# Optimization experiments

Measured on AMD Instinct MI355X. Metric: run time of the kernel, lower is better.

Reference implementation:

```python
import jax, jax.numpy as jnp
import numpy as np

N_PATCHES = 4
PATCH = 64  # image_size // n_patches = 256 // 4
GROUPS = 32
EPS = 1e-5


def setup_inputs() -> dict:
    key = jax.random.key(0)
    k1, k2 = jax.random.split(key)
    x = jax.random.normal(k1, (8, 128, 256, 256), dtype=jnp.float32)
    y = jax.random.normal(k2, (8, 128, 256, 256), dtype=jnp.float32)
    # GroupNorm affine params (torch default init: weight=1, bias=0)
    weight = jnp.ones((128,), dtype=jnp.float32)
    bias = jnp.zeros((128,), dtype=jnp.float32)
    return {"x": x, "y": y, "weight": weight, "bias": bias}


def reference(x, y, weight, bias):
    b, c, h, w = x.shape
    n, p, g = N_PATCHES, PATCH, GROUPS
    cg = c // g
    # extract patches: (b, c, n, p, n, p) -> (b, i, j, c, hp, wp)
    xp = x.reshape(b, c, n, p, n, p).transpose(0, 2, 4, 1, 3, 5)
    yp = y.reshape(b, c, n, p, n, p).transpose(0, 2, 4, 1, 3, 5)
    # per-patch GroupNorm in float32 (GroupNorm.forward casts to float)
    xg = xp.astype(jnp.float32).reshape(b, n, n, g, cg, p, p)
    mean = xg.mean(axis=(4, 5, 6), keepdims=True)
    var = xg.var(axis=(4, 5, 6), keepdims=True)
    xn = (xg - mean) * jax.lax.rsqrt(var + EPS)
    xn = xn.reshape(b, n, n, c, p, p)
    xn = xn * weight[:, None, None] + bias[:, None, None]
    xn = xn.astype(x.dtype)
    # silu-gated scale, shift = 0
    out = xn * (1.0 + jax.nn.silu(yp))
    # reassemble: (b, i, j, c, hp, wp) -> (b, c, i, hp, j, wp) -> (b, c, H, W)
    out = out.transpose(0, 3, 1, 4, 2, 5).reshape(b, c, h, w)
    return out
```

## Files before the change

### kernel.cpp

```cpp
#include <hip/hip_runtime.h>


constexpr int CHANNELS = 128;
constexpr int HW = 256;
constexpr int NP = 4;
constexpr int G = 32;
constexpr int CPG = CHANNELS / G;
constexpr float EPS = 1e-5f;

typedef float f32x4 __attribute__((ext_vector_type(4)));

__device__ __forceinline__ float fast_gate(float v) {
    const float e = __builtin_amdgcn_exp2f(v * -1.44269504088896f);
    return 1.0f + v * __builtin_amdgcn_rcpf(1.0f + e);
}

__global__ __launch_bounds__(512, 4)
void gn_patch_gate_kernel(const float* __restrict__ x,
                          const float* __restrict__ y,
                          const float* __restrict__ wgt,
                          const float* __restrict__ bvec,
                          float* __restrict__ out)
{
    __shared__ float4 xs[4096];
    __shared__ float red[16];

    const int bid = blockIdx.x;
    const int g  = bid & 31;
    const int pj = (bid >> 5) & 3;
    const int pi = (bid >> 7) & 3;
    const int b  = bid >> 9;
    const int tid = threadIdx.x;

    const unsigned cstride = HW * HW;
    const unsigned base =
        (((unsigned)b * CHANNELS + (unsigned)g * CPG) * HW + (unsigned)pi * 64) * HW
        + (unsigned)pj * 64;

    float y0[8], y1[8], y2[8], y3[8];
    unsigned addr[8];
    float s = 0.f, ss = 0.f;
#pragma unroll
    for (int k = 0; k < 8; ++k) {
        const unsigned u  = (unsigned)tid + (unsigned)(k << 9);
        const unsigned cc = u >> 10;
        const unsigned r  = (u >> 4) & 63;
        const unsigned c4 = u & 15;
        const unsigned a  = base + cc * cstride + r * HW + (c4 << 2);
        addr[k] = a;
        const float4 v = *reinterpret_cast<const float4*>(x + a);
        const float4 w = *reinterpret_cast<const float4*>(y + a);
        float w0 = w.x, w1 = w.y, w2 = w.z, w3 = w.w;
        asm volatile("" : "+v"(w0), "+v"(w1), "+v"(w2), "+v"(w3));
        y0[k] = w0; y1[k] = w1; y2[k] = w2; y3[k] = w3;
        xs[u] = v;
        s  += (v.x + v.y) + (v.z + v.w);
        ss += (v.x * v.x + v.y * v.y) + (v.z * v.z + v.w * v.w);
    }

#pragma unroll
    for (int off = 32; off; off >>= 1) {
        s  += __shfl_xor(s, off);
        ss += __shfl_xor(ss, off);
    }
    const int wv = tid >> 6;
    if ((tid & 63) == 0) { red[wv] = s; red[8 + wv] = ss; }
    __syncthreads();
    float ts = 0.f, tss = 0.f;
#pragma unroll
    for (int q = 0; q < 8; ++q) { ts += red[q]; tss += red[8 + q]; }

    const float inv_n = 1.0f / 16384.0f;
    const float mean = ts * inv_n;
    const float var  = fmaxf(tss * inv_n - mean * mean, 0.f);
    const float rstd = rsqrtf(var + EPS);

    float scl[CPG], sft[CPG];
#pragma unroll
    for (int cc = 0; cc < CPG; ++cc) {
        const float wc = wgt[g * CPG + cc];
        scl[cc] = wc * rstd;
        sft[cc] = bvec[g * CPG + cc] - mean * rstd * wc;
    }

#pragma unroll
    for (int k = 0; k < 8; ++k) {
        const unsigned u  = (unsigned)tid + (unsigned)(k << 9);
        const unsigned cc = u >> 10;
        const float4 v  = xs[u];
        f32x4 o;
        o.x = (v.x * scl[cc] + sft[cc]) * fast_gate(y0[k]);
        o.y = (v.y * scl[cc] + sft[cc]) * fast_gate(y1[k]);
        o.z = (v.z * scl[cc] + sft[cc]) * fast_gate(y2[k]);
        o.w = (v.w * scl[cc] + sft[cc]) * fast_gate(y3[k]);
        __builtin_nontemporal_store(o, reinterpret_cast<f32x4*>(out + addr[k]));
    }
}

extern "C" void kernel_launch(void* const* d_in, const int* in_sizes, int n_in,
                              void* d_out, int out_size, void* d_ws, size_t ws_size,
                              hipStream_t stream) {
    const float* x    = (const float*)d_in[0];
    const float* y    = (const float*)d_in[1];
    const float* wgt  = (const float*)d_in[2];
    const float* bvec = (const float*)d_in[3];
    float* out = (float*)d_out;

    const int B = in_sizes[0] / (CHANNELS * HW * HW);
    const int nblocks = B * NP * NP * G;
    gn_patch_gate_kernel<<<dim3(nblocks), dim3(512), 0, stream>>>(x, y, wgt, bvec, out);
}
```

Measured before the change: 151.5 us.

## Drop LDS staging; re-read x from cache in second pass, raise occupancy

Result: slower. 158.6 us (+4.7%).

```diff
diff --git a/kernel.cpp b/kernel.cpp
--- a/kernel.cpp
+++ b/kernel.cpp
@@ -15,14 +15,13 @@
     return 1.0f + v * __builtin_amdgcn_rcpf(1.0f + e);
 }
 
-__global__ __launch_bounds__(512, 4)
+__global__ __launch_bounds__(512, 8)
 void gn_patch_gate_kernel(const float* __restrict__ x,
                           const float* __restrict__ y,
                           const float* __restrict__ wgt,
                           const float* __restrict__ bvec,
                           float* __restrict__ out)
 {
-    __shared__ float4 xs[4096];
     __shared__ float red[16];
 
     const int bid = blockIdx.x;
@@ -36,24 +35,13 @@
     const unsigned base =
         (((unsigned)b * CHANNELS + (unsigned)g * CPG) * HW + (unsigned)pi * 64) * HW
         + (unsigned)pj * 64;
+    const unsigned a0 = base + (((unsigned)tid >> 4) << 8) + (((unsigned)tid & 15) << 2);
 
-    float y0[8], y1[8], y2[8], y3[8];
-    unsigned addr[8];
     float s = 0.f, ss = 0.f;
 #pragma unroll
     for (int k = 0; k < 8; ++k) {
-        const unsigned u  = (unsigned)tid + (unsigned)(k << 9);
-        const unsigned cc = u >> 10;
-        const unsigned r  = (u >> 4) & 63;
-        const unsigned c4 = u & 15;
-        const unsigned a  = base + cc * cstride + r * HW + (c4 << 2);
-        addr[k] = a;
+        const unsigned a = a0 + (unsigned)((k >> 1) * 65536 + (k & 1) * 8192);
         const float4 v = *reinterpret_cast<const float4*>(x + a);
-        const float4 w = *reinterpret_cast<const float4*>(y + a);
-        float w0 = w.x, w1 = w.y, w2 = w.z, w3 = w.w;
-        asm volatile("" : "+v"(w0), "+v"(w1), "+v"(w2), "+v"(w3));
-        y0[k] = w0; y1[k] = w1; y2[k] = w2; y3[k] = w3;
-        xs[u] = v;
         s  += (v.x + v.y) + (v.z + v.w);
         ss += (v.x * v.x + v.y * v.y) + (v.z * v.z + v.w * v.w);
     }
@@ -85,15 +73,16 @@
 
 #pragma unroll
     for (int k = 0; k < 8; ++k) {
-        const unsigned u  = (unsigned)tid + (unsigned)(k << 9);
-        const unsigned cc = u >> 10;
-        const float4 v  = xs[u];
+        const unsigned a = a0 + (unsigned)((k >> 1) * 65536 + (k & 1) * 8192);
+        const int cc = k >> 1;
+        const float4 v = *reinterpret_cast<const float4*>(x + a);
+        const float4 w = *reinterpret_cast<const float4*>(y + a);
         f32x4 o;
-        o.x = (v.x * scl[cc] + sft[cc]) * fast_gate(y0[k]);
-        o.y = (v.y * scl[cc] + sft[cc]) * fast_gate(y1[k]);
-        o.z = (v.z * scl[cc] + sft[cc]) * fast_gate(y2[k]);
-        o.w = (v.w * scl[cc] + sft[cc]) * fast_gate(y3[k]);
-        __builtin_nontemporal_store(o, reinterpret_cast<f32x4*>(out + addr[k]));
+        o.x = (v.x * scl[cc] + sft[cc]) * fast_gate(w.x);
+        o.y = (v.y * scl[cc] + sft[cc]) * fast_gate(w.y);
+        o.z = (v.z * scl[cc] + sft[cc]) * fast_gate(w.z);
+        o.w = (v.w * scl[cc] + sft[cc]) * fast_gate(w.w);
+        __builtin_nontemporal_store(o, reinterpret_cast<f32x4*>(out + a));
     }
 }
 
```
